# Kernel tuning notes

Hardware: AMD Instinct MI355X
Metric: run time of the kernel (lower is better)

The kernel has to match this reference:

```python
import jax, jax.numpy as jnp
import numpy as np

N = 100000
E = 6400000
GAMMA = 1.0
SUPPORT = 0.05


def cohesion_kernel(q, h):
    # piecewise Akinci cohesion kernel (Cd normalization is unused in the original)
    qm1_3_q3 = (q - 1.0) ** 3 * q ** 3
    k1 = 128.0 * qm1_3_q3 + 1.0   # q <= 0.5
    k2 = 64.0 * qm1_3_q3           # q > 0.5
    return -jnp.where(q <= 0.5, k1, k2)


def kernel_gradient(q, dist, h):
    # 2D Wendland C2 kernel gradient: W = 7/(pi h^2) (1-q)^4 (1+4q)
    C = 7.0 / (np.pi * h ** 2)
    dWdq = C * (-20.0 * q * jnp.clip(1.0 - q, 0.0, None) ** 3) / h
    return dWdq[:, None] * dist  # [E,2]


def setup_inputs() -> dict:
    key = jax.random.key(0)
    k1, k2, k3, k4, k5, k6, k7 = jax.random.split(key, 7)
    neighbors = jnp.stack([
        jax.random.randint(k1, (E,), 0, N),
        jax.random.randint(k2, (E,), 0, N),
    ], axis=0)  # [2,E] int
    fluidAreas = jax.random.uniform(k3, (N,), dtype=jnp.float32)
    fluidDensities = jax.random.uniform(k4, (N,), dtype=jnp.float32) + 0.5  # avoid div-by-0
    fluidRestDensity = jax.random.uniform(k5, (N,), dtype=jnp.float32) + 0.5
    fluidRadialDistances = jax.random.uniform(k6, (E,), dtype=jnp.float32)  # q in [0,1]
    fluidDistances = jax.random.normal(k7, (E, 2), dtype=jnp.float32)
    # normalize to unit direction vectors as in the SPH pipeline
    fluidDistances = fluidDistances / (jnp.linalg.norm(fluidDistances, axis=1, keepdims=True) + 1e-7)
    return {
        'neighbors': neighbors,
        'fluidAreas': fluidAreas,
        'fluidDensities': fluidDensities,
        'fluidRestDensity': fluidRestDensity,
        'fluidRadialDistances': fluidRadialDistances,
        'fluidDistances': fluidDistances,
    }


def reference(neighbors, fluidAreas, fluidDensities, fluidRestDensity,
              fluidRadialDistances, fluidDistances):
    i = neighbors[0]
    j = neighbors[1]

    # computeNormalFunction
    fac_n = fluidAreas[j] / fluidDensities[j]                  # [E]
    grad = kernel_gradient(fluidRadialDistances, fluidDistances, SUPPORT)  # [E,2]
    normals = SUPPORT * jax.ops.segment_sum(fac_n[:, None] * grad, i, num_segments=N)  # [N,2]

    # computeCurvatureForce
    curvature = -GAMMA * jax.ops.segment_sum(normals[i] - normals[j], i, num_segments=N)

    # computeCohesionForce
    fac_c = fluidAreas[j] * fluidRestDensity[j]                # [E]
    kern = cohesion_kernel(fluidRadialDistances, SUPPORT)      # [E]
    cohesion = -GAMMA * jax.ops.segment_sum((fac_c * kern)[:, None] * fluidDistances, i, num_segments=N)

    # both forces are accumulated into fluidAcceleration
    return curvature + cohesion
```

## Files before the change

kernel.cpp:

```cpp
#include <hip/hip_runtime.h>

constexpr int N_PART = 100000;
constexpr int N_EDGE = 6400000;
constexpr float SUPPORT = 0.05f;
constexpr float PI_F = 3.14159265358979323846f;

constexpr int CH_LOG2 = 12;
constexpr int CH      = 1 << CH_LOG2;
constexpr int NCH     = (N_EDGE + CH - 1) / CH;
constexpr int BIN_LOG2 = 13;
constexpr int BINSZ   = 1 << BIN_LOG2;
constexpr int NBIN    = (N_PART + BINSZ - 1) / BINSZ;
constexpr int G_MAX   = 39;
constexpr int ST_NW   = 8;

__global__ __launch_bounds__(512) void l1_sort(
    const int* __restrict__ nb,
    const float* __restrict__ areas,
    const float* __restrict__ dens,
    const float* __restrict__ rest,
    const float* __restrict__ q,
    const float2* __restrict__ dist,
    unsigned* __restrict__ gpack,
    float2* __restrict__ gpay1,
    float2* __restrict__ gpay2,
    unsigned* __restrict__ btab)
{
    __shared__ unsigned rec_pack[CH];
    __shared__ float    rec_q[CH];
    __shared__ float    rec_dx[CH];
    __shared__ float    rec_dy[CH];
    __shared__ unsigned hist[ST_NW * NBIN];
    __shared__ unsigned curw[ST_NW * NBIN];
    __shared__ unsigned base[NBIN + 1];

    const int t   = blockIdx.x;
    const int c0  = t * CH;
    const int len = min(CH, N_EDGE - c0);
    const int tid = threadIdx.x;
    const int wid = tid >> 6;

    for (int k = tid; k < ST_NW * NBIN; k += 512) hist[k] = 0u;
    __syncthreads();

    for (int idx = tid; idx < len; idx += 512) {
        unsigned i = (unsigned)nb[c0 + idx];
        atomicAdd(&hist[wid * NBIN + (i >> BIN_LOG2)], 1u);
    }
    __syncthreads();

    if (tid == 0) {
        unsigned run = 0;
        for (int b = 0; b < NBIN; ++b) {
            base[b] = run;
            for (int w = 0; w < ST_NW; ++w) {
                curw[w * NBIN + b] = run;
                run += hist[w * NBIN + b];
            }
        }
        base[NBIN] = run;
    }
    __syncthreads();
    if (tid < NBIN)  btab[t * 16 + tid]  = base[tid];
    if (tid == NBIN) btab[t * 16 + NBIN] = (unsigned)len;

    for (int idx = tid; idx < len; idx += 512) {
        unsigned i = (unsigned)nb[c0 + idx];
        unsigned j = (unsigned)nb[N_EDGE + c0 + idx];
        float   qq = q[c0 + idx];
        float2  d  = dist[c0 + idx];
        unsigned bin = i >> BIN_LOG2;
        unsigned r = atomicAdd(&curw[wid * NBIN + bin], 1u) & (CH - 1);
        rec_pack[r] = ((i & (BINSZ - 1)) << 17) | j;
        rec_q[r]    = qq;
        rec_dx[r]   = d.x;
        rec_dy[r]   = d.y;
    }
    __syncthreads();

    const float Cw = 7.0f / (PI_F * SUPPORT * SUPPORT);
    for (int p = tid; p < len; p += 512) {
        unsigned pack = rec_pack[p];
        float qq = rec_q[p];
        float dx = rec_dx[p], dy = rec_dy[p];
        unsigned j = pack & 0x1FFFFu;

        float omq  = fmaxf(1.0f - qq, 0.0f);
        float dWdq = Cw * (-20.0f * qq * omq * omq * omq) * (1.0f / SUPPORT);
        float s    = SUPPORT * (areas[j] / dens[j]) * dWdq;

        float qm1  = qq - 1.0f;
        float tt   = qm1 * qm1 * qm1 * qq * qq * qq;
        float kern = (qq <= 0.5f) ? fmaf(128.0f, tt, 1.0f) : 64.0f * tt;
        float fc   = areas[j] * rest[j] * kern;

        int o = c0 + p;
        gpack[o] = pack;
        gpay1[o] = make_float2(s * dx, s * dy);
        gpay2[o] = make_float2(fc * dx, fc * dy);
    }
}

__global__ __launch_bounds__(512) void passB(
    const unsigned* __restrict__ btab,
    const unsigned* __restrict__ gpack,
    const float2* __restrict__ gpay1,
    float2* __restrict__ partials,
    int G)
{
    __shared__ float accx[BINSZ];
    __shared__ float accy[BINSZ];
    const int b = blockIdx.x % NBIN;
    const int g = blockIdx.x / NBIN;
    const int wave = threadIdx.x >> 6;
    const int lane = threadIdx.x & 63;

    for (int k = threadIdx.x; k < BINSZ; k += 512) { accx[k] = 0.0f; accy[k] = 0.0f; }
    __syncthreads();

    const int t0 = (int)((long long)g * NCH / G);
    const int t1 = (int)((long long)(g + 1) * NCH / G);
    for (int t = t0 + wave; t < t1; t += 8) {
        const int c0  = t * CH;
        const unsigned ln = min(btab[t * 16 + NBIN], (unsigned)CH);
        unsigned sb = min(btab[t * 16 + b], ln);
        unsigned se = min(btab[t * 16 + b + 1], ln);
        for (unsigned k = sb + lane; k < se; k += 64) {
            int o = c0 + (int)k;
            unsigned pk = gpack[o];
            float2 p = gpay1[o];
            unsigned loc = (pk >> 17) & (BINSZ - 1);
            atomicAdd(&accx[loc], p.x);
            atomicAdd(&accy[loc], p.y);
        }
    }
    __syncthreads();

    float2* __restrict__ dst = partials + (size_t)g * (NBIN * BINSZ) + (size_t)b * BINSZ;
    for (int k = threadIdx.x; k < BINSZ; k += 512)
        dst[k] = make_float2(accx[k], accy[k]);
}

__global__ __launch_bounds__(512) void passD(
    const unsigned* __restrict__ btab,
    const unsigned* __restrict__ gpack,
    const float2* __restrict__ gpay2,
    const float2* __restrict__ normals,
    float2* __restrict__ partials,
    int G)
{
    __shared__ float accx[BINSZ];
    __shared__ float accy[BINSZ];
    const int b = blockIdx.x % NBIN;
    const int g = blockIdx.x / NBIN;
    const int wave = threadIdx.x >> 6;
    const int lane = threadIdx.x & 63;

    for (int k = threadIdx.x; k < BINSZ; k += 512) { accx[k] = 0.0f; accy[k] = 0.0f; }
    __syncthreads();

    const int gbase = b * BINSZ;
    const int t0 = (int)((long long)g * NCH / G);
    const int t1 = (int)((long long)(g + 1) * NCH / G);
    for (int t = t0 + wave; t < t1; t += 8) {
        const int c0  = t * CH;
        const unsigned ln = min(btab[t * 16 + NBIN], (unsigned)CH);
        unsigned sb = min(btab[t * 16 + b], ln);
        unsigned se = min(btab[t * 16 + b + 1], ln);
        for (unsigned k = sb + lane; k < se; k += 64) {
            int o = c0 + (int)k;
            unsigned pk = gpack[o];
            float2 coh = gpay2[o];
            unsigned loc = (pk >> 17) & (BINSZ - 1);
            unsigned j   = min(pk & 0x1FFFFu, (unsigned)(N_PART - 1));
            unsigned ii  = min((unsigned)(gbase + loc), (unsigned)(N_PART - 1));
            float2 nj = normals[j];
            float2 ni = normals[ii];
            atomicAdd(&accx[loc], nj.x - ni.x + coh.x);
            atomicAdd(&accy[loc], nj.y - ni.y + coh.y);
        }
    }
    __syncthreads();

    float2* __restrict__ dst = partials + (size_t)g * (NBIN * BINSZ) + (size_t)b * BINSZ;
    for (int k = threadIdx.x; k < BINSZ; k += 512)
        dst[k] = make_float2(accx[k], accy[k]);
}

__global__ __launch_bounds__(256) void reduceG(
    const float2* __restrict__ partials, float2* __restrict__ dst, int G)
{
    int p = blockIdx.x * blockDim.x + threadIdx.x;
    if (p >= N_PART) return;
    float ax = 0.0f, ay = 0.0f;
    for (int g = 0; g < G; ++g) {
        float2 v = partials[(size_t)g * (NBIN * BINSZ) + p];
        ax += v.x; ay += v.y;
    }
    dst[p] = make_float2(ax, ay);
}

constexpr int FB_BSZ_LOG2 = 13;
constexpr int FB_BSZ   = 1 << FB_BSZ_LOG2;
constexpr int FB_NBINS = (N_PART + FB_BSZ - 1) / FB_BSZ;
constexpr int FB_NP_PAD = FB_NBINS * FB_BSZ;
constexpr int FB_C_TARGET = 39;

__global__ __launch_bounds__(1024) void fb_pass1_binned(
    const int* __restrict__ nb, const float* __restrict__ areas,
    const float* __restrict__ dens, const float* __restrict__ q,
    const float2* __restrict__ dist, float* __restrict__ partials, int C)
{
    __shared__ float lds[2 * FB_BSZ];
    const int b = blockIdx.x % FB_NBINS;
    const int c = blockIdx.x / FB_NBINS;
    for (int k = threadIdx.x; k < 2 * FB_BSZ; k += blockDim.x) lds[k] = 0.0f;
    __syncthreads();
    const int start = (int)((long long)c       * (N_EDGE / 4) / C) * 4;
    const int end   = (int)((long long)(c + 1) * (N_EDGE / 4) / C) * 4;
    const int4* __restrict__ nb4 = (const int4*)nb;
    const float Cw = 7.0f / (PI_F * SUPPORT * SUPPORT);
    for (int e = start + (int)threadIdx.x * 4; e < end; e += (int)blockDim.x * 4) {
        int4 iq = nb4[e >> 2];
        #pragma unroll
        for (int k = 0; k < 4; ++k) {
            int iv = (k == 0) ? iq.x : (k == 1) ? iq.y : (k == 2) ? iq.z : iq.w;
            if ((iv >> FB_BSZ_LOG2) == b) {
                int ee = e + k;
                int j  = nb[N_EDGE + ee];
                float qq  = q[ee];
                float fac = areas[j] / dens[j];
                float omq  = fmaxf(1.0f - qq, 0.0f);
                float dWdq = Cw * (-20.0f * qq * omq * omq * omq) * (1.0f / SUPPORT);
                float s = SUPPORT * fac * dWdq;
                float2 d = dist[ee];
                int loc = (iv & (FB_BSZ - 1)) << 1;
                atomicAdd(&lds[loc],     s * d.x);
                atomicAdd(&lds[loc + 1], s * d.y);
            }
        }
    }
    __syncthreads();
    float2* __restrict__ dst = (float2*)partials + (size_t)c * FB_NP_PAD + (size_t)b * FB_BSZ;
    const float2* __restrict__ src = (const float2*)lds;
    for (int k = threadIdx.x; k < FB_BSZ; k += blockDim.x) dst[k] = src[k];
}

__global__ __launch_bounds__(1024) void fb_pass2_binned(
    const int* __restrict__ nb, const float* __restrict__ areas,
    const float* __restrict__ rest, const float* __restrict__ q,
    const float2* __restrict__ dist, const float2* __restrict__ normals,
    float* __restrict__ partials, int C)
{
    __shared__ float lds[2 * FB_BSZ];
    const int b = blockIdx.x % FB_NBINS;
    const int c = blockIdx.x / FB_NBINS;
    for (int k = threadIdx.x; k < 2 * FB_BSZ; k += blockDim.x) lds[k] = 0.0f;
    __syncthreads();
    const int start = (int)((long long)c       * (N_EDGE / 4) / C) * 4;
    const int end   = (int)((long long)(c + 1) * (N_EDGE / 4) / C) * 4;
    const int4* __restrict__ nb4 = (const int4*)nb;
    for (int e = start + (int)threadIdx.x * 4; e < end; e += (int)blockDim.x * 4) {
        int4 iq = nb4[e >> 2];
        #pragma unroll
        for (int k = 0; k < 4; ++k) {
            int iv = (k == 0) ? iq.x : (k == 1) ? iq.y : (k == 2) ? iq.z : iq.w;
            if ((iv >> FB_BSZ_LOG2) == b) {
                int ee = e + k;
                int j  = nb[N_EDGE + ee];
                float2 ni = normals[iv];
                float2 nj = normals[j];
                float qq  = q[ee];
                float fc  = areas[j] * rest[j];
                float qm1 = qq - 1.0f;
                float t   = qm1 * qm1 * qm1 * qq * qq * qq;
                float kern = (qq <= 0.5f) ? fmaf(128.0f, t, 1.0f) : 64.0f * t;
                float2 d = dist[ee];
                int loc = (iv & (FB_BSZ - 1)) << 1;
                atomicAdd(&lds[loc],     -(ni.x - nj.x) + fc * kern * d.x);
                atomicAdd(&lds[loc + 1], -(ni.y - nj.y) + fc * kern * d.y);
            }
        }
    }
    __syncthreads();
    float2* __restrict__ dst = (float2*)partials + (size_t)c * FB_NP_PAD + (size_t)b * FB_BSZ;
    const float2* __restrict__ src = (const float2*)lds;
    for (int k = threadIdx.x; k < FB_BSZ; k += blockDim.x) dst[k] = src[k];
}

__global__ __launch_bounds__(256) void fb_reduce_partials(
    const float* __restrict__ partials, float* __restrict__ dst, int C)
{
    int p = blockIdx.x * blockDim.x + threadIdx.x;
    if (p >= N_PART) return;
    const float2* __restrict__ p2 = (const float2*)partials;
    float ax = 0.0f, ay = 0.0f;
    for (int c = 0; c < C; ++c) {
        float2 v = p2[(size_t)c * FB_NP_PAD + p];
        ax += v.x; ay += v.y;
    }
    ((float2*)dst)[p] = make_float2(ax, ay);
}

__global__ __launch_bounds__(256) void fb_zero2(float* __restrict__ a,
                                                float* __restrict__ b, int n) {
    int idx = blockIdx.x * blockDim.x + threadIdx.x;
    if (idx < n) { a[idx] = 0.0f; b[idx] = 0.0f; }
}

__global__ __launch_bounds__(256) void fb_pass1_atomic(
    const int* __restrict__ nb, const float* __restrict__ areas,
    const float* __restrict__ dens, const float* __restrict__ q,
    const float2* __restrict__ dist, float* __restrict__ normals)
{
    int e = blockIdx.x * blockDim.x + threadIdx.x;
    if (e >= N_EDGE) return;
    int i = nb[e];
    int j = nb[N_EDGE + e];
    float qq  = q[e];
    float fac = areas[j] / dens[j];
    const float Cw = 7.0f / (PI_F * SUPPORT * SUPPORT);
    float omq  = fmaxf(1.0f - qq, 0.0f);
    float dWdq = Cw * (-20.0f * qq * omq * omq * omq) * (1.0f / SUPPORT);
    float s = SUPPORT * fac * dWdq;
    float2 d = dist[e];
    atomicAdd(&normals[2 * i],     s * d.x);
    atomicAdd(&normals[2 * i + 1], s * d.y);
}

__global__ __launch_bounds__(256) void fb_pass2_atomic(
    const int* __restrict__ nb, const float* __restrict__ areas,
    const float* __restrict__ rest, const float* __restrict__ q,
    const float2* __restrict__ dist, const float2* __restrict__ normals,
    float* __restrict__ out)
{
    int e = blockIdx.x * blockDim.x + threadIdx.x;
    if (e >= N_EDGE) return;
    int i = nb[e];
    int j = nb[N_EDGE + e];
    float2 ni = normals[i];
    float2 nj = normals[j];
    float qq  = q[e];
    float fc  = areas[j] * rest[j];
    float qm1 = qq - 1.0f;
    float t   = qm1 * qm1 * qm1 * qq * qq * qq;
    float kern = (qq <= 0.5f) ? fmaf(128.0f, t, 1.0f) : 64.0f * t;
    float2 d = dist[e];
    atomicAdd(&out[2 * i],     -(ni.x - nj.x) + fc * kern * d.x);
    atomicAdd(&out[2 * i + 1], -(ni.y - nj.y) + fc * kern * d.y);
}

extern "C" void kernel_launch(void* const* d_in, const int* in_sizes, int n_in,
                              void* d_out, int out_size, void* d_ws, size_t ws_size,
                              hipStream_t stream) {
    const int*   nb    = (const int*)d_in[0];
    const float* areas = (const float*)d_in[1];
    const float* dens  = (const float*)d_in[2];
    const float* rest  = (const float*)d_in[3];
    const float* q     = (const float*)d_in[4];
    const float* dist  = (const float*)d_in[5];
    float* out = (float*)d_out;

    size_t off = 0;
    auto take = [&](size_t bytes) { size_t o = off; off += (bytes + 255) & ~(size_t)255; return o; };
    size_t o_pack    = take((size_t)N_EDGE * sizeof(unsigned));
    size_t o_pay1    = take((size_t)N_EDGE * sizeof(float2));
    size_t o_pay2    = take((size_t)N_EDGE * sizeof(float2));
    size_t o_btab    = take((size_t)NCH * 16 * sizeof(unsigned));
    size_t o_normals = take((size_t)N_PART * sizeof(float2));
    size_t base_need = off;
    const size_t per_g = (size_t)(NBIN * BINSZ) * sizeof(float2);

    int G = 0;
    if (ws_size > base_need) {
        G = (int)((ws_size - base_need) / per_g);
        if (G > G_MAX) G = G_MAX;
    }

    char* ws = (char*)d_ws;

    if (G >= 6) {
        unsigned* gpack   = (unsigned*)(ws + o_pack);
        float2*   gpay1   = (float2*)(ws + o_pay1);
        float2*   gpay2   = (float2*)(ws + o_pay2);
        unsigned* btab    = (unsigned*)(ws + o_btab);
        float2*   normals = (float2*)(ws + o_normals);
        float2*   partials= (float2*)(ws + base_need);

        l1_sort<<<NCH, 512, 0, stream>>>(
            nb, areas, dens, rest, q, (const float2*)dist,
            gpack, gpay1, gpay2, btab);
        passB<<<NBIN * G, 512, 0, stream>>>(btab, gpack, gpay1, partials, G);
        reduceG<<<(N_PART + 255) / 256, 256, 0, stream>>>(partials, normals, G);
        passD<<<NBIN * G, 512, 0, stream>>>(btab, gpack, gpay2, normals, partials, G);
        reduceG<<<(N_PART + 255) / 256, 256, 0, stream>>>(partials, (float2*)out, G);
        return;
    }

    const size_t normals_pad = 1 << 20;
    float* normals  = (float*)d_ws;
    float* partials = (float*)((char*)d_ws + normals_pad);
    const size_t per_chunk = (size_t)FB_NP_PAD * 2 * sizeof(float);
    int C = 0;
    if (ws_size > normals_pad) {
        C = (int)((ws_size - normals_pad) / per_chunk);
        if (C > FB_C_TARGET) C = FB_C_TARGET;
    }

    if (C >= 4) {
        const int grid = FB_NBINS * C;
        fb_pass1_binned<<<grid, 1024, 0, stream>>>(
            nb, areas, dens, q, (const float2*)dist, partials, C);
        fb_reduce_partials<<<(N_PART + 255) / 256, 256, 0, stream>>>(partials, normals, C);
        fb_pass2_binned<<<grid, 1024, 0, stream>>>(
            nb, areas, rest, q, (const float2*)dist, (const float2*)normals, partials, C);
        fb_reduce_partials<<<(N_PART + 255) / 256, 256, 0, stream>>>(partials, out, C);
    } else {
        const int nv = 2 * N_PART;
        fb_zero2<<<(nv + 255) / 256, 256, 0, stream>>>(normals, out, nv);
        const int blocks = (N_EDGE + 255) / 256;
        fb_pass1_atomic<<<blocks, 256, 0, stream>>>(
            nb, areas, dens, q, (const float2*)dist, normals);
        fb_pass2_atomic<<<blocks, 256, 0, stream>>>(
            nb, areas, rest, q, (const float2*)dist, (const float2*)normals, out);
    }
}
```

Before: 432.2 us.

## Precompute per-particle factors and load edge chunk once into registers in sort

Adds a small kernel that precomputes areas/dens and areas*rest per particle into a packed float2 table, so the sort kernel does one 8-byte gather per edge instead of three scalar gathers plus a division. The sort kernel now loads each edge's i, j, q and direction into registers once, rather than reading the neighbor index twice across two passes. The per-bin prefix scan is also parallelized across threads instead of being done serially by one thread. The costs are an extra kernel launch, more register pressure from holding eight edges per thread, and additional workspace for the factor table.

Result: faster. 373.9 us (-13.5%).

```diff
diff --git a/kernel.cpp b/kernel.cpp
--- a/kernel.cpp
+++ b/kernel.cpp
@@ -14,11 +14,20 @@
 constexpr int G_MAX   = 39;
 constexpr int ST_NW   = 8;
 
-__global__ __launch_bounds__(512) void l1_sort(
-    const int* __restrict__ nb,
+__global__ __launch_bounds__(512) void prep_fac(
     const float* __restrict__ areas,
     const float* __restrict__ dens,
     const float* __restrict__ rest,
+    float2* __restrict__ fac)
+{
+    int p = blockIdx.x * blockDim.x + threadIdx.x;
+    if (p < N_PART)
+        fac[p] = make_float2(areas[p] / dens[p], areas[p] * rest[p]);
+}
+
+__global__ __launch_bounds__(512) void l1_sort(
+    const int* __restrict__ nb,
+    const float2* __restrict__ fac,
     const float* __restrict__ q,
     const float2* __restrict__ dist,
     unsigned* __restrict__ gpack,
@@ -33,6 +42,7 @@
     __shared__ unsigned hist[ST_NW * NBIN];
     __shared__ unsigned curw[ST_NW * NBIN];
     __shared__ unsigned base[NBIN + 1];
+    __shared__ unsigned bcnt[NBIN];
 
     const int t   = blockIdx.x;
     const int c0  = t * CH;
@@ -41,40 +51,63 @@
     const int wid = tid >> 6;
 
     for (int k = tid; k < ST_NW * NBIN; k += 512) hist[k] = 0u;
-    __syncthreads();
-
-    for (int idx = tid; idx < len; idx += 512) {
-        unsigned i = (unsigned)nb[c0 + idx];
-        atomicAdd(&hist[wid * NBIN + (i >> BIN_LOG2)], 1u);
-    }
-    __syncthreads();
-
+
+    unsigned iv[8], jv[8];
+    float    qv[8], dxv[8], dyv[8];
+    #pragma unroll
+    for (int k = 0; k < 8; ++k) {
+        int idx = tid + k * 512;
+        if (idx < len) {
+            iv[k] = (unsigned)nb[c0 + idx];
+            jv[k] = (unsigned)nb[N_EDGE + c0 + idx];
+            qv[k] = q[c0 + idx];
+            float2 d = dist[c0 + idx];
+            dxv[k] = d.x;
+            dyv[k] = d.y;
+        }
+    }
+    __syncthreads();
+
+    #pragma unroll
+    for (int k = 0; k < 8; ++k) {
+        int idx = tid + k * 512;
+        if (idx < len)
+            atomicAdd(&hist[wid * NBIN + (iv[k] >> BIN_LOG2)], 1u);
+    }
+    __syncthreads();
+
+    if (tid < NBIN) {
+        unsigned run = 0;
+        for (int w = 0; w < ST_NW; ++w) {
+            curw[w * NBIN + tid] = run;
+            run += hist[w * NBIN + tid];
+        }
+        bcnt[tid] = run;
+    }
+    __syncthreads();
     if (tid == 0) {
         unsigned run = 0;
-        for (int b = 0; b < NBIN; ++b) {
-            base[b] = run;
-            for (int w = 0; w < ST_NW; ++w) {
-                curw[w * NBIN + b] = run;
-                run += hist[w * NBIN + b];
-            }
-        }
+        for (int b = 0; b < NBIN; ++b) { base[b] = run; run += bcnt[b]; }
         base[NBIN] = run;
     }
     __syncthreads();
+    if (tid < ST_NW * NBIN) curw[tid] += base[tid % NBIN];
     if (tid < NBIN)  btab[t * 16 + tid]  = base[tid];
     if (tid == NBIN) btab[t * 16 + NBIN] = (unsigned)len;
-
-    for (int idx = tid; idx < len; idx += 512) {
-        unsigned i = (unsigned)nb[c0 + idx];
-        unsigned j = (unsigned)nb[N_EDGE + c0 + idx];
-        float   qq = q[c0 + idx];
-        float2  d  = dist[c0 + idx];
-        unsigned bin = i >> BIN_LOG2;
-        unsigned r = atomicAdd(&curw[wid * NBIN + bin], 1u) & (CH - 1);
-        rec_pack[r] = ((i & (BINSZ - 1)) << 17) | j;
-        rec_q[r]    = qq;
-        rec_dx[r]   = d.x;
-        rec_dy[r]   = d.y;
+    __syncthreads();
+
+    #pragma unroll
+    for (int k = 0; k < 8; ++k) {
+        int idx = tid + k * 512;
+        if (idx < len) {
+            unsigned i   = iv[k];
+            unsigned bin = i >> BIN_LOG2;
+            unsigned r = atomicAdd(&curw[wid * NBIN + bin], 1u) & (CH - 1);
+            rec_pack[r] = ((i & (BINSZ - 1)) << 17) | jv[k];
+            rec_q[r]    = qv[k];
+            rec_dx[r]   = dxv[k];
+            rec_dy[r]   = dyv[k];
+        }
     }
     __syncthreads();
 
@@ -84,15 +117,16 @@
         float qq = rec_q[p];
         float dx = rec_dx[p], dy = rec_dy[p];
         unsigned j = pack & 0x1FFFFu;
+        float2 f = fac[j];
 
         float omq  = fmaxf(1.0f - qq, 0.0f);
         float dWdq = Cw * (-20.0f * qq * omq * omq * omq) * (1.0f / SUPPORT);
-        float s    = SUPPORT * (areas[j] / dens[j]) * dWdq;
+        float s    = SUPPORT * f.x * dWdq;
 
         float qm1  = qq - 1.0f;
         float tt   = qm1 * qm1 * qm1 * qq * qq * qq;
         float kern = (qq <= 0.5f) ? fmaf(128.0f, tt, 1.0f) : 64.0f * tt;
-        float fc   = areas[j] * rest[j] * kern;
+        float fc   = f.y * kern;
 
         int o = c0 + p;
         gpack[o] = pack;
@@ -368,6 +402,7 @@
     size_t o_pay2    = take((size_t)N_EDGE * sizeof(float2));
     size_t o_btab    = take((size_t)NCH * 16 * sizeof(unsigned));
     size_t o_normals = take((size_t)N_PART * sizeof(float2));
+    size_t o_fac     = take((size_t)N_PART * sizeof(float2));
     size_t base_need = off;
     const size_t per_g = (size_t)(NBIN * BINSZ) * sizeof(float2);
 
@@ -385,10 +420,12 @@
         float2*   gpay2   = (float2*)(ws + o_pay2);
         unsigned* btab    = (unsigned*)(ws + o_btab);
         float2*   normals = (float2*)(ws + o_normals);
+        float2*   fac     = (float2*)(ws + o_fac);
         float2*   partials= (float2*)(ws + base_need);
 
+        prep_fac<<<(N_PART + 511) / 512, 512, 0, stream>>>(areas, dens, rest, fac);
         l1_sort<<<NCH, 512, 0, stream>>>(
-            nb, areas, dens, rest, q, (const float2*)dist,
+            nb, fac, q, (const float2*)dist,
             gpack, gpay1, gpay2, btab);
         passB<<<NBIN * G, 512, 0, stream>>>(btab, gpack, gpay1, partials, G);
         reduceG<<<(N_PART + 255) / 256, 256, 0, stream>>>(partials, normals, G);
```

## Replace bin-sorted LDS reduction with flat global atomic scatter passes

Applied to the files above, without the earlier changes.

Drops the chunk-sort plus per-bin LDS accumulation pipeline and its partial-sum reductions. In their place come two flat edge passes, each thread handling 8 edges with vectorized loads, that scatter directly into global normals and output using unsafeAtomicAdd. A small prep kernel precomputes per-particle area/density and area*rest factors and zeroes the accumulators. This removes the intermediate edge payload writes and reads and the partials traffic, but relies on hardware float atomics to global memory with random addresses, and the summation order becomes nondeterministic.

New measurement: 1.396 ms. +222.9%, slower.

```diff
diff --git a/kernel.cpp b/kernel.cpp
--- a/kernel.cpp
+++ b/kernel.cpp
@@ -5,301 +5,122 @@
 constexpr float SUPPORT = 0.05f;
 constexpr float PI_F = 3.14159265358979323846f;
 
-constexpr int CH_LOG2 = 12;
-constexpr int CH      = 1 << CH_LOG2;
-constexpr int NCH     = (N_EDGE + CH - 1) / CH;
-constexpr int BIN_LOG2 = 13;
-constexpr int BINSZ   = 1 << BIN_LOG2;
-constexpr int NBIN    = (N_PART + BINSZ - 1) / BINSZ;
-constexpr int G_MAX   = 39;
-constexpr int ST_NW   = 8;
-
-__global__ __launch_bounds__(512) void l1_sort(
-    const int* __restrict__ nb,
+
+__device__ __forceinline__ void gAdd(float* p, float v) {
+#if defined(__HIP_PLATFORM_AMD__) || defined(__HIP_PLATFORM_HCC__)
+    unsafeAtomicAdd(p, v);
+#else
+    atomicAdd(p, v);
+#endif
+}
+
+__global__ __launch_bounds__(256) void prep_zero(
     const float* __restrict__ areas,
     const float* __restrict__ dens,
     const float* __restrict__ rest,
+    float2* __restrict__ fac,
+    float2* __restrict__ normals,
+    float2* __restrict__ out)
+{
+    int p = blockIdx.x * blockDim.x + threadIdx.x;
+    if (p < N_PART) {
+        fac[p]     = make_float2(areas[p] / dens[p], areas[p] * rest[p]);
+        normals[p] = make_float2(0.0f, 0.0f);
+        out[p]     = make_float2(0.0f, 0.0f);
+    }
+}
+
+__global__ __launch_bounds__(256) void flat_pass1(
+    const int* __restrict__ nb,
+    const float2* __restrict__ fac,
     const float* __restrict__ q,
-    const float2* __restrict__ dist,
-    unsigned* __restrict__ gpack,
-    float2* __restrict__ gpay1,
-    float2* __restrict__ gpay2,
-    unsigned* __restrict__ btab)
-{
-    __shared__ unsigned rec_pack[CH];
-    __shared__ float    rec_q[CH];
-    __shared__ float    rec_dx[CH];
-    __shared__ float    rec_dy[CH];
-    __shared__ unsigned hist[ST_NW * NBIN];
-    __shared__ unsigned curw[ST_NW * NBIN];
-    __shared__ unsigned base[NBIN + 1];
-
-    const int t   = blockIdx.x;
-    const int c0  = t * CH;
-    const int len = min(CH, N_EDGE - c0);
-    const int tid = threadIdx.x;
-    const int wid = tid >> 6;
-
-    for (int k = tid; k < ST_NW * NBIN; k += 512) hist[k] = 0u;
-    __syncthreads();
-
-    for (int idx = tid; idx < len; idx += 512) {
-        unsigned i = (unsigned)nb[c0 + idx];
-        atomicAdd(&hist[wid * NBIN + (i >> BIN_LOG2)], 1u);
-    }
-    __syncthreads();
-
-    if (tid == 0) {
-        unsigned run = 0;
-        for (int b = 0; b < NBIN; ++b) {
-            base[b] = run;
-            for (int w = 0; w < ST_NW; ++w) {
-                curw[w * NBIN + b] = run;
-                run += hist[w * NBIN + b];
-            }
-        }
-        base[NBIN] = run;
-    }
-    __syncthreads();
-    if (tid < NBIN)  btab[t * 16 + tid]  = base[tid];
-    if (tid == NBIN) btab[t * 16 + NBIN] = (unsigned)len;
-
-    for (int idx = tid; idx < len; idx += 512) {
-        unsigned i = (unsigned)nb[c0 + idx];
-        unsigned j = (unsigned)nb[N_EDGE + c0 + idx];
-        float   qq = q[c0 + idx];
-        float2  d  = dist[c0 + idx];
-        unsigned bin = i >> BIN_LOG2;
-        unsigned r = atomicAdd(&curw[wid * NBIN + bin], 1u) & (CH - 1);
-        rec_pack[r] = ((i & (BINSZ - 1)) << 17) | j;
-        rec_q[r]    = qq;
-        rec_dx[r]   = d.x;
-        rec_dy[r]   = d.y;
-    }
-    __syncthreads();
-
-    const float Cw = 7.0f / (PI_F * SUPPORT * SUPPORT);
-    for (int p = tid; p < len; p += 512) {
-        unsigned pack = rec_pack[p];
-        float qq = rec_q[p];
-        float dx = rec_dx[p], dy = rec_dy[p];
-        unsigned j = pack & 0x1FFFFu;
-
-        float omq  = fmaxf(1.0f - qq, 0.0f);
-        float dWdq = Cw * (-20.0f * qq * omq * omq * omq) * (1.0f / SUPPORT);
-        float s    = SUPPORT * (areas[j] / dens[j]) * dWdq;
-
-        float qm1  = qq - 1.0f;
-        float tt   = qm1 * qm1 * qm1 * qq * qq * qq;
+    const float* __restrict__ dist,
+    float* __restrict__ norm)
+{
+    const int t = blockIdx.x * blockDim.x + threadIdx.x;
+    const int e8 = t * 8;
+    if (e8 >= N_EDGE) return;
+
+    const int4*   nbi4 = (const int4*)nb;
+    const int4*   nbj4 = (const int4*)(nb + N_EDGE);
+    const float4* q4   = (const float4*)q;
+    const float4* d4   = (const float4*)dist;
+
+    int4   ia = nbi4[2 * t],     ib = nbi4[2 * t + 1];
+    int4   ja = nbj4[2 * t],     jb = nbj4[2 * t + 1];
+    float4 qa = q4[2 * t],       qb = q4[2 * t + 1];
+    float4 dA = d4[4 * t], dB = d4[4 * t + 1], dC = d4[4 * t + 2], dD = d4[4 * t + 3];
+
+    const float Cm20 = -20.0f * 7.0f / (PI_F * SUPPORT * SUPPORT);
+
+    int   iv[8] = { ia.x, ia.y, ia.z, ia.w, ib.x, ib.y, ib.z, ib.w };
+    int   jv[8] = { ja.x, ja.y, ja.z, ja.w, jb.x, jb.y, jb.z, jb.w };
+    float qv[8] = { qa.x, qa.y, qa.z, qa.w, qb.x, qb.y, qb.z, qb.w };
+    float dx[8] = { dA.x, dA.z, dB.x, dB.z, dC.x, dC.z, dD.x, dD.z };
+    float dy[8] = { dA.y, dA.w, dB.y, dB.w, dC.y, dC.w, dD.y, dD.w };
+
+    float fx[8];
+    #pragma unroll
+    for (int k = 0; k < 8; ++k)
+        fx[k] = fac[jv[k]].x;
+
+    #pragma unroll
+    for (int k = 0; k < 8; ++k) {
+        float qq  = qv[k];
+        float omq = fmaxf(1.0f - qq, 0.0f);
+        float s   = fx[k] * Cm20 * qq * omq * omq * omq;
+        gAdd(&norm[2 * iv[k]],     s * dx[k]);
+        gAdd(&norm[2 * iv[k] + 1], s * dy[k]);
+    }
+}
+
+__global__ __launch_bounds__(256) void flat_pass2(
+    const int* __restrict__ nb,
+    const float2* __restrict__ fac,
+    const float* __restrict__ q,
+    const float* __restrict__ dist,
+    const float2* __restrict__ normals,
+    float* __restrict__ out)
+{
+    const int t = blockIdx.x * blockDim.x + threadIdx.x;
+    const int e8 = t * 8;
+    if (e8 >= N_EDGE) return;
+
+    const int4*   nbi4 = (const int4*)nb;
+    const int4*   nbj4 = (const int4*)(nb + N_EDGE);
+    const float4* q4   = (const float4*)q;
+    const float4* d4   = (const float4*)dist;
+
+    int4   ia = nbi4[2 * t],     ib = nbi4[2 * t + 1];
+    int4   ja = nbj4[2 * t],     jb = nbj4[2 * t + 1];
+    float4 qa = q4[2 * t],       qb = q4[2 * t + 1];
+    float4 dA = d4[4 * t], dB = d4[4 * t + 1], dC = d4[4 * t + 2], dD = d4[4 * t + 3];
+
+    int   iv[8] = { ia.x, ia.y, ia.z, ia.w, ib.x, ib.y, ib.z, ib.w };
+    int   jv[8] = { ja.x, ja.y, ja.z, ja.w, jb.x, jb.y, jb.z, jb.w };
+    float qv[8] = { qa.x, qa.y, qa.z, qa.w, qb.x, qb.y, qb.z, qb.w };
+    float dx[8] = { dA.x, dA.z, dB.x, dB.z, dC.x, dC.z, dD.x, dD.z };
+    float dy[8] = { dA.y, dA.w, dB.y, dB.w, dC.y, dC.w, dD.y, dD.w };
+
+    float  fy[8];
+    float2 nj[8], ni[8];
+    #pragma unroll
+    for (int k = 0; k < 8; ++k) {
+        fy[k] = fac[jv[k]].y;
+        nj[k] = normals[jv[k]];
+        ni[k] = normals[iv[k]];
+    }
+
+    #pragma unroll
+    for (int k = 0; k < 8; ++k) {
+        float qq  = qv[k];
+        float qm1 = qq - 1.0f;
+        float tt  = qm1 * qm1 * qm1 * qq * qq * qq;
         float kern = (qq <= 0.5f) ? fmaf(128.0f, tt, 1.0f) : 64.0f * tt;
-        float fc   = areas[j] * rest[j] * kern;
-
-        int o = c0 + p;
-        gpack[o] = pack;
-        gpay1[o] = make_float2(s * dx, s * dy);
-        gpay2[o] = make_float2(fc * dx, fc * dy);
-    }
-}
-
-__global__ __launch_bounds__(512) void passB(
-    const unsigned* __restrict__ btab,
-    const unsigned* __restrict__ gpack,
-    const float2* __restrict__ gpay1,
-    float2* __restrict__ partials,
-    int G)
-{
-    __shared__ float accx[BINSZ];
-    __shared__ float accy[BINSZ];
-    const int b = blockIdx.x % NBIN;
-    const int g = blockIdx.x / NBIN;
-    const int wave = threadIdx.x >> 6;
-    const int lane = threadIdx.x & 63;
-
-    for (int k = threadIdx.x; k < BINSZ; k += 512) { accx[k] = 0.0f; accy[k] = 0.0f; }
-    __syncthreads();
-
-    const int t0 = (int)((long long)g * NCH / G);
-    const int t1 = (int)((long long)(g + 1) * NCH / G);
-    for (int t = t0 + wave; t < t1; t += 8) {
-        const int c0  = t * CH;
-        const unsigned ln = min(btab[t * 16 + NBIN], (unsigned)CH);
-        unsigned sb = min(btab[t * 16 + b], ln);
-        unsigned se = min(btab[t * 16 + b + 1], ln);
-        for (unsigned k = sb + lane; k < se; k += 64) {
-            int o = c0 + (int)k;
-            unsigned pk = gpack[o];
-            float2 p = gpay1[o];
-            unsigned loc = (pk >> 17) & (BINSZ - 1);
-            atomicAdd(&accx[loc], p.x);
-            atomicAdd(&accy[loc], p.y);
-        }
-    }
-    __syncthreads();
-
-    float2* __restrict__ dst = partials + (size_t)g * (NBIN * BINSZ) + (size_t)b * BINSZ;
-    for (int k = threadIdx.x; k < BINSZ; k += 512)
-        dst[k] = make_float2(accx[k], accy[k]);
-}
-
-__global__ __launch_bounds__(512) void passD(
-    const unsigned* __restrict__ btab,
-    const unsigned* __restrict__ gpack,
-    const float2* __restrict__ gpay2,
-    const float2* __restrict__ normals,
-    float2* __restrict__ partials,
-    int G)
-{
-    __shared__ float accx[BINSZ];
-    __shared__ float accy[BINSZ];
-    const int b = blockIdx.x % NBIN;
-    const int g = blockIdx.x / NBIN;
-    const int wave = threadIdx.x >> 6;
-    const int lane = threadIdx.x & 63;
-
-    for (int k = threadIdx.x; k < BINSZ; k += 512) { accx[k] = 0.0f; accy[k] = 0.0f; }
-    __syncthreads();
-
-    const int gbase = b * BINSZ;
-    const int t0 = (int)((long long)g * NCH / G);
-    const int t1 = (int)((long long)(g + 1) * NCH / G);
-    for (int t = t0 + wave; t < t1; t += 8) {
-        const int c0  = t * CH;
-        const unsigned ln = min(btab[t * 16 + NBIN], (unsigned)CH);
-        unsigned sb = min(btab[t * 16 + b], ln);
-        unsigned se = min(btab[t * 16 + b + 1], ln);
-        for (unsigned k = sb + lane; k < se; k += 64) {
-            int o = c0 + (int)k;
-            unsigned pk = gpack[o];
-            float2 coh = gpay2[o];
-            unsigned loc = (pk >> 17) & (BINSZ - 1);
-            unsigned j   = min(pk & 0x1FFFFu, (unsigned)(N_PART - 1));
-            unsigned ii  = min((unsigned)(gbase + loc), (unsigned)(N_PART - 1));
-            float2 nj = normals[j];
-            float2 ni = normals[ii];
-            atomicAdd(&accx[loc], nj.x - ni.x + coh.x);
-            atomicAdd(&accy[loc], nj.y - ni.y + coh.y);
-        }
-    }
-    __syncthreads();
-
-    float2* __restrict__ dst = partials + (size_t)g * (NBIN * BINSZ) + (size_t)b * BINSZ;
-    for (int k = threadIdx.x; k < BINSZ; k += 512)
-        dst[k] = make_float2(accx[k], accy[k]);
-}
-
-__global__ __launch_bounds__(256) void reduceG(
-    const float2* __restrict__ partials, float2* __restrict__ dst, int G)
-{
-    int p = blockIdx.x * blockDim.x + threadIdx.x;
-    if (p >= N_PART) return;
-    float ax = 0.0f, ay = 0.0f;
-    for (int g = 0; g < G; ++g) {
-        float2 v = partials[(size_t)g * (NBIN * BINSZ) + p];
-        ax += v.x; ay += v.y;
-    }
-    dst[p] = make_float2(ax, ay);
-}
-
-constexpr int FB_BSZ_LOG2 = 13;
-constexpr int FB_BSZ   = 1 << FB_BSZ_LOG2;
-constexpr int FB_NBINS = (N_PART + FB_BSZ - 1) / FB_BSZ;
-constexpr int FB_NP_PAD = FB_NBINS * FB_BSZ;
-constexpr int FB_C_TARGET = 39;
-
-__global__ __launch_bounds__(1024) void fb_pass1_binned(
-    const int* __restrict__ nb, const float* __restrict__ areas,
-    const float* __restrict__ dens, const float* __restrict__ q,
-    const float2* __restrict__ dist, float* __restrict__ partials, int C)
-{
-    __shared__ float lds[2 * FB_BSZ];
-    const int b = blockIdx.x % FB_NBINS;
-    const int c = blockIdx.x / FB_NBINS;
-    for (int k = threadIdx.x; k < 2 * FB_BSZ; k += blockDim.x) lds[k] = 0.0f;
-    __syncthreads();
-    const int start = (int)((long long)c       * (N_EDGE / 4) / C) * 4;
-    const int end   = (int)((long long)(c + 1) * (N_EDGE / 4) / C) * 4;
-    const int4* __restrict__ nb4 = (const int4*)nb;
-    const float Cw = 7.0f / (PI_F * SUPPORT * SUPPORT);
-    for (int e = start + (int)threadIdx.x * 4; e < end; e += (int)blockDim.x * 4) {
-        int4 iq = nb4[e >> 2];
-        #pragma unroll
-        for (int k = 0; k < 4; ++k) {
-            int iv = (k == 0) ? iq.x : (k == 1) ? iq.y : (k == 2) ? iq.z : iq.w;
-            if ((iv >> FB_BSZ_LOG2) == b) {
-                int ee = e + k;
-                int j  = nb[N_EDGE + ee];
-                float qq  = q[ee];
-                float fac = areas[j] / dens[j];
-                float omq  = fmaxf(1.0f - qq, 0.0f);
-                float dWdq = Cw * (-20.0f * qq * omq * omq * omq) * (1.0f / SUPPORT);
-                float s = SUPPORT * fac * dWdq;
-                float2 d = dist[ee];
-                int loc = (iv & (FB_BSZ - 1)) << 1;
-                atomicAdd(&lds[loc],     s * d.x);
-                atomicAdd(&lds[loc + 1], s * d.y);
-            }
-        }
-    }
-    __syncthreads();
-    float2* __restrict__ dst = (float2*)partials + (size_t)c * FB_NP_PAD + (size_t)b * FB_BSZ;
-    const float2* __restrict__ src = (const float2*)lds;
-    for (int k = threadIdx.x; k < FB_BSZ; k += blockDim.x) dst[k] = src[k];
-}
-
-__global__ __launch_bounds__(1024) void fb_pass2_binned(
-    const int* __restrict__ nb, const float* __restrict__ areas,
-    const float* __restrict__ rest, const float* __restrict__ q,
-    const float2* __restrict__ dist, const float2* __restrict__ normals,
-    float* __restrict__ partials, int C)
-{
-    __shared__ float lds[2 * FB_BSZ];
-    const int b = blockIdx.x % FB_NBINS;
-    const int c = blockIdx.x / FB_NBINS;
-    for (int k = threadIdx.x; k < 2 * FB_BSZ; k += blockDim.x) lds[k] = 0.0f;
-    __syncthreads();
-    const int start = (int)((long long)c       * (N_EDGE / 4) / C) * 4;
-    const int end   = (int)((long long)(c + 1) * (N_EDGE / 4) / C) * 4;
-    const int4* __restrict__ nb4 = (const int4*)nb;
-    for (int e = start + (int)threadIdx.x * 4; e < end; e += (int)blockDim.x * 4) {
-        int4 iq = nb4[e >> 2];
-        #pragma unroll
-        for (int k = 0; k < 4; ++k) {
-            int iv = (k == 0) ? iq.x : (k == 1) ? iq.y : (k == 2) ? iq.z : iq.w;
-            if ((iv >> FB_BSZ_LOG2) == b) {
-                int ee = e + k;
-                int j  = nb[N_EDGE + ee];
-                float2 ni = normals[iv];
-                float2 nj = normals[j];
-                float qq  = q[ee];
-                float fc  = areas[j] * rest[j];
-                float qm1 = qq - 1.0f;
-                float t   = qm1 * qm1 * qm1 * qq * qq * qq;
-                float kern = (qq <= 0.5f) ? fmaf(128.0f, t, 1.0f) : 64.0f * t;
-                float2 d = dist[ee];
-                int loc = (iv & (FB_BSZ - 1)) << 1;
-                atomicAdd(&lds[loc],     -(ni.x - nj.x) + fc * kern * d.x);
-                atomicAdd(&lds[loc + 1], -(ni.y - nj.y) + fc * kern * d.y);
-            }
-        }
-    }
-    __syncthreads();
-    float2* __restrict__ dst = (float2*)partials + (size_t)c * FB_NP_PAD + (size_t)b * FB_BSZ;
-    const float2* __restrict__ src = (const float2*)lds;
-    for (int k = threadIdx.x; k < FB_BSZ; k += blockDim.x) dst[k] = src[k];
-}
-
-__global__ __launch_bounds__(256) void fb_reduce_partials(
-    const float* __restrict__ partials, float* __restrict__ dst, int C)
-{
-    int p = blockIdx.x * blockDim.x + threadIdx.x;
-    if (p >= N_PART) return;
-    const float2* __restrict__ p2 = (const float2*)partials;
-    float ax = 0.0f, ay = 0.0f;
-    for (int c = 0; c < C; ++c) {
-        float2 v = p2[(size_t)c * FB_NP_PAD + p];
-        ax += v.x; ay += v.y;
-    }
-    ((float2*)dst)[p] = make_float2(ax, ay);
+        float fc  = fy[k] * kern;
+        gAdd(&out[2 * iv[k]],     nj[k].x - ni[k].x + fc * dx[k]);
+        gAdd(&out[2 * iv[k] + 1], nj[k].y - ni[k].y + fc * dy[k]);
+    }
 }
 
 __global__ __launch_bounds__(256) void fb_zero2(float* __restrict__ a,
@@ -363,65 +184,34 @@
 
     size_t off = 0;
     auto take = [&](size_t bytes) { size_t o = off; off += (bytes + 255) & ~(size_t)255; return o; };
-    size_t o_pack    = take((size_t)N_EDGE * sizeof(unsigned));
-    size_t o_pay1    = take((size_t)N_EDGE * sizeof(float2));
-    size_t o_pay2    = take((size_t)N_EDGE * sizeof(float2));
-    size_t o_btab    = take((size_t)NCH * 16 * sizeof(unsigned));
+    size_t o_fac     = take((size_t)N_PART * sizeof(float2));
     size_t o_normals = take((size_t)N_PART * sizeof(float2));
     size_t base_need = off;
-    const size_t per_g = (size_t)(NBIN * BINSZ) * sizeof(float2);
-
-    int G = 0;
-    if (ws_size > base_need) {
-        G = (int)((ws_size - base_need) / per_g);
-        if (G > G_MAX) G = G_MAX;
-    }
 
     char* ws = (char*)d_ws;
 
-    if (G >= 6) {
-        unsigned* gpack   = (unsigned*)(ws + o_pack);
-        float2*   gpay1   = (float2*)(ws + o_pay1);
-        float2*   gpay2   = (float2*)(ws + o_pay2);
-        unsigned* btab    = (unsigned*)(ws + o_btab);
-        float2*   normals = (float2*)(ws + o_normals);
-        float2*   partials= (float2*)(ws + base_need);
-
-        l1_sort<<<NCH, 512, 0, stream>>>(
-            nb, areas, dens, rest, q, (const float2*)dist,
-            gpack, gpay1, gpay2, btab);
-        passB<<<NBIN * G, 512, 0, stream>>>(btab, gpack, gpay1, partials, G);
-        reduceG<<<(N_PART + 255) / 256, 256, 0, stream>>>(partials, normals, G);
-        passD<<<NBIN * G, 512, 0, stream>>>(btab, gpack, gpay2, normals, partials, G);
-        reduceG<<<(N_PART + 255) / 256, 256, 0, stream>>>(partials, (float2*)out, G);
+    if (ws_size >= base_need) {
+        float2* fac     = (float2*)(ws + o_fac);
+        float2* normals = (float2*)(ws + o_normals);
+
+        prep_zero<<<(N_PART + 255) / 256, 256, 0, stream>>>(
+            areas, dens, rest, fac, normals, (float2*)out);
+
+        const int nthreads = N_EDGE / 8;
+        const int nblocks  = (nthreads + 255) / 256;
+        flat_pass1<<<nblocks, 256, 0, stream>>>(
+            nb, fac, q, dist, (float*)normals);
+        flat_pass2<<<nblocks, 256, 0, stream>>>(
+            nb, fac, q, dist, normals, out);
         return;
     }
 
-    const size_t normals_pad = 1 << 20;
-    float* normals  = (float*)d_ws;
-    float* partials = (float*)((char*)d_ws + normals_pad);
-    const size_t per_chunk = (size_t)FB_NP_PAD * 2 * sizeof(float);
-    int C = 0;
-    if (ws_size > normals_pad) {
-        C = (int)((ws_size - normals_pad) / per_chunk);
-        if (C > FB_C_TARGET) C = FB_C_TARGET;
-    }
-
-    if (C >= 4) {
-        const int grid = FB_NBINS * C;
-        fb_pass1_binned<<<grid, 1024, 0, stream>>>(
-            nb, areas, dens, q, (const float2*)dist, partials, C);
-        fb_reduce_partials<<<(N_PART + 255) / 256, 256, 0, stream>>>(partials, normals, C);
-        fb_pass2_binned<<<grid, 1024, 0, stream>>>(
-            nb, areas, rest, q, (const float2*)dist, (const float2*)normals, partials, C);
-        fb_reduce_partials<<<(N_PART + 255) / 256, 256, 0, stream>>>(partials, out, C);
-    } else {
-        const int nv = 2 * N_PART;
-        fb_zero2<<<(nv + 255) / 256, 256, 0, stream>>>(normals, out, nv);
-        const int blocks = (N_EDGE + 255) / 256;
-        fb_pass1_atomic<<<blocks, 256, 0, stream>>>(
-            nb, areas, dens, q, (const float2*)dist, normals);
-        fb_pass2_atomic<<<blocks, 256, 0, stream>>>(
-            nb, areas, rest, q, (const float2*)dist, (const float2*)normals, out);
-    }
-}
+    float* normals = (float*)d_ws;
+    const int nv = 2 * N_PART;
+    fb_zero2<<<(nv + 255) / 256, 256, 0, stream>>>(normals, out, nv);
+    const int blocks = (N_EDGE + 255) / 256;
+    fb_pass1_atomic<<<blocks, 256, 0, stream>>>(
+        nb, areas, dens, q, (const float2*)dist, normals);
+    fb_pass2_atomic<<<blocks, 256, 0, stream>>>(
+        nb, areas, rest, q, (const float2*)dist, (const float2*)normals, out);
+}
```
